# Optimization experiments

Hardware: AMD Instinct MI355X
Metric: run time of the kernel (lower is better)

The kernel has to match this reference:

```python
import jax, jax.numpy as jnp
import numpy as np

B, T, E, H, R, NTAGS, V = 128, 24, 512, 512, 512, 400, 20000

def setup_inputs() -> dict:
    key = jax.random.key(0)
    ks = jax.random.split(key, 12)
    sc = 0.03  # xavier-ish scale for 512-dim mats
    return {
        'captions': jax.random.randint(ks[0], (B, T), 0, V),
        'encoder_tags': jax.random.uniform(ks[1], (B, NTAGS), jnp.float32),
        'h0': jax.random.normal(ks[2], (2, B, H), jnp.float32),
        'c0': jax.random.normal(ks[3], (2, B, H), jnp.float32),
        'Wa': jax.random.normal(ks[4], (4, E, R), jnp.float32) * sc,
        'Wb': jax.random.normal(ks[5], (4, NTAGS, R), jnp.float32) * sc,
        'Wc': jax.random.normal(ks[6], (4, R, H), jnp.float32) * sc,
        'Ua': jax.random.normal(ks[7], (4, H, R), jnp.float32) * sc,
        'Ub': jax.random.normal(ks[8], (4, NTAGS, R), jnp.float32) * sc,
        'Uc': jax.random.normal(ks[9], (4, R, H), jnp.float32) * sc,
        'b': jnp.zeros((4, H), jnp.float32),
        'emb': jax.random.normal(ks[10], (V, E), jnp.float32) * 0.02,
        'Wout': jax.random.normal(ks[11], (H, V), jnp.float32) * sc,
        'bout': jnp.zeros((V,), jnp.float32),
    }


def reference(captions, encoder_tags, h0, c0, Wa, Wb, Wc, Ua, Ub, Uc, b, emb, Wout, bout):
    # Training branch of SCNAttnDecoder.forward_fn with teacher_forcing_ratio=1.0,
    # dropout in eval mode (identity). Gate order along leading axis 4: (i, f, o, c~).
    s = encoder_tags                                      # [B, NTAGS]
    temp2 = jnp.einsum('bt,gtr->gbr', s, Wb)              # precompute_mats: s @ Wb_*
    temp5 = jnp.einsum('bt,gtr->gbr', s, Ub)              # s @ Ub_*
    # Decoder inputs: zeros at t=0, then embedded ground-truth tokens (teacher forcing)
    emb_caps = emb[captions]                              # [B, T, E]
    xs = jnp.concatenate([jnp.zeros((captions.shape[0], 1, emb.shape[1]), emb.dtype),
                          emb_caps[:, :-1]], axis=1)
    xs = jnp.swapaxes(xs, 0, 1)                           # [T, B, E]
    # Initial state: last encoder layer, forward direction
    h_init, c_init = h0[0], c0[0]                         # [B, H]

    def step(carry, x):
        h, c = carry
        temp1 = jnp.einsum('be,ger->gbr', x, Wa)          # decoder_input @ Wa_*
        temp6 = jnp.einsum('bh,ghr->gbr', h, Ua)          # rnn_h @ Ua_*
        gx = jnp.einsum('gbr,grh->gbh', temp1 * temp2, Wc)
        gh = jnp.einsum('gbr,grh->gbh', temp5 * temp6, Uc)
        pre = gx + gh + b[:, None, :]                     # [4, B, H]
        i = jax.nn.sigmoid(pre[0])
        f = jax.nn.sigmoid(pre[1])
        o = jax.nn.sigmoid(pre[2])
        ct = jnp.tanh(pre[3])
        c_new = f * c + i * ct
        h_new = o * jnp.tanh(c_new)
        return (h_new, c_new), h_new

    (_, _), hs = jax.lax.scan(step, (h_init, c_init), xs)  # hs: [T, B, H]
    logits = jnp.einsum('tbh,hv->tbv', hs, Wout) + bout     # out Linear
    return jnp.swapaxes(logits, 0, 1)                       # [B, T, V]
```

## Files before the change

### kernel.cpp

```cpp
#include <hip/hip_runtime.h>
#include <hip/hip_bf16.h>
#include <math.h>

typedef unsigned short u16;
typedef short short8 __attribute__((ext_vector_type(8)));
typedef float floatx4 __attribute__((ext_vector_type(4)));

#define NB 128
#define NT 24
#define NE 512
#define NH 512
#define NR 512
#define NTAG 400
#define NV 20000

__device__ __forceinline__ float bfu(u16 u) {
    unsigned x = ((unsigned)u) << 16;
    return __builtin_bit_cast(float, x);
}
__device__ __forceinline__ u16 f2b(float f) {
    unsigned u = __builtin_bit_cast(unsigned, f);
    unsigned r = (u + 0x7FFFu + ((u >> 16) & 1u)) >> 16;
    return (u16)r;
}
__device__ __forceinline__ float ldin(const void* p, long i, int f32) {
    return f32 ? ((const float*)p)[i] : bfu(((const u16*)p)[i]);
}

__global__ __launch_bounds__(256) void k_detect(const void* emb, int* flag) {
    __shared__ int cnt;
    if (threadIdx.x == 0) cnt = 0;
    __syncthreads();
    const u16* p = (const u16*)emb;
    int local = 0;
    for (int i = threadIdx.x; i < 65536; i += 256) {
        if ((p[i] & 0x7F80) == 0x7F80) local++;
    }
    atomicAdd(&cnt, local);
    __syncthreads();
    if (threadIdx.x == 0) *flag = (cnt > 4) ? 1 : 0;
}

__global__ __launch_bounds__(256) void k_tags(const void* __restrict__ s,
        const void* __restrict__ Wb, const void* __restrict__ Ub,
        const int* __restrict__ flagp, float* __restrict__ temp2, float* __restrict__ temp5,
        int* __restrict__ flags) {
    if (blockIdx.x == 0 && threadIdx.x < 256) flags[threadIdx.x] = 0;
    int f32 = *flagp;
    int idx = blockIdx.x * 256 + threadIdx.x;
    int r = idx & (NR - 1);
    int gb = idx >> 9;
    int b = gb & (NB - 1);
    int g = gb >> 7;
    float a2 = 0.f, a5 = 0.f;
    if (f32) {
        const float* srow = (const float*)s + b * NTAG;
        const float* wb = (const float*)Wb + (long)g * NTAG * NR + r;
        const float* ub = (const float*)Ub + (long)g * NTAG * NR + r;
        for (int t = 0; t < NTAG; t++) {
            float sv = srow[t];
            a2 += sv * wb[(long)t * NR];
            a5 += sv * ub[(long)t * NR];
        }
    } else {
        const u16* srow = (const u16*)s + b * NTAG;
        const u16* wb = (const u16*)Wb + (long)g * NTAG * NR + r;
        const u16* ub = (const u16*)Ub + (long)g * NTAG * NR + r;
        for (int t = 0; t < NTAG; t++) {
            float sv = bfu(srow[t]);
            a2 += sv * bfu(wb[(long)t * NR]);
            a5 += sv * bfu(ub[(long)t * NR]);
        }
    }
    temp2[idx] = a2;
    temp5[idx] = a5;
}

__global__ __launch_bounds__(256) void k_tr(const void* __restrict__ Ua,
        const void* __restrict__ Uc, const int* __restrict__ flagp,
        u16* __restrict__ UaS, u16* __restrict__ UcS) {
    int f32 = *flagp;
    int z = blockIdx.z;
    int which = z >> 2, g = z & 3;
    const void* src = which ? Uc : Ua;
    u16* dst = which ? UcS : UaS;
    __shared__ u16 tile[64][65];
    int i0 = blockIdx.x * 64;
    int j0 = blockIdx.y * 64;
    int t = threadIdx.x;
    int il = t >> 2, js = (t & 3) * 16;
    long base = ((long)g * 512 + i0 + il) * 512 + j0 + js;
    if (f32) {
        const float* q = (const float*)src + base;
        #pragma unroll
        for (int j = 0; j < 16; j++) tile[il][js + j] = f2b(q[j]);
    } else {
        const u16* q = (const u16*)src + base;
        #pragma unroll
        for (int j = 0; j < 16; j++) tile[il][js + j] = q[j];
    }
    __syncthreads();
    #pragma unroll
    for (int h = 0; h < 2; h++) {
        int idx = t + h * 256;
        int kl = idx >> 6, rl = idx & 63;
        u16 outv[8] __attribute__((aligned(16)));
        #pragma unroll
        for (int j = 0; j < 8; j++) outv[j] = tile[kl * 8 + j][rl];
        long ob = ((long)(g * 64 + (i0 >> 3) + kl) * 512 + (j0 + rl)) * 8;
        *(uint4*)(dst + ob) = *(uint4*)outv;
    }
}

template<int MODE>
__global__ __launch_bounds__(256) void k_mfma(const void* __restrict__ Asrc,
        const void* __restrict__ Bsrc, void* __restrict__ dst,
        const int* __restrict__ captions, const float* __restrict__ temp2,
        const void* __restrict__ bout, const int* __restrict__ flagp) {
    const int f32 = *flagp;
    const int bm = blockIdx.x * 64;
    const int bn = blockIdx.y * 128;
    const int g = blockIdx.z;
    const int NN = (MODE == 2) ? NV : NR;
    const int ldb = (MODE == 2) ? NV : NR;
    __shared__ __align__(16) u16 As[64 * 40];
    __shared__ __align__(16) u16 Bs[32 * 132];
    const int tid = threadIdx.x;
    const int sam = tid >> 2, sak = (tid & 3) * 8;
    const int sbk = tid >> 3, sbn = (tid & 7) * 16;
    long arow = 0;
    int azero = 0;
    if (MODE == 0) {
        int mg = bm + sam, tt = mg >> 7, bb = mg & (NB - 1);
        if (tt == 0) azero = 1;
        else arow = (long)captions[bb * NT + tt - 1] * NE;
    } else if (MODE == 1) {
        arow = ((long)g * NT * NB + bm + sam) * NR;
    } else {
        arow = (long)(bm + sam) * NH;
    }
    long bbase;
    if (MODE == 2) bbase = bn + sbn;
    else bbase = (long)g * 512 * 512 + bn + sbn;
    const int bguard = (MODE == 2) && (bn + 128 > NN);

    const int wv = tid >> 6, ln = tid & 63;
    const int q = ln >> 4, l15 = ln & 15;
    floatx4 acc[4][2];
    #pragma unroll
    for (int i = 0; i < 4; i++)
        #pragma unroll
        for (int j = 0; j < 2; j++)
            #pragma unroll
            for (int r = 0; r < 4; r++) acc[i][j][r] = 0.f;

    for (int k0 = 0; k0 < 512; k0 += 32) {
        u16 ta[8] __attribute__((aligned(16)));
        if (MODE == 0) {
            if (azero) {
                #pragma unroll
                for (int j = 0; j < 8; j++) ta[j] = 0;
            } else if (f32) {
                const float* qa = (const float*)Asrc + arow + k0 + sak;
                #pragma unroll
                for (int j = 0; j < 8; j++) ta[j] = f2b(qa[j]);
            } else {
                *(uint4*)ta = *(const uint4*)((const u16*)Asrc + arow + k0 + sak);
            }
        } else {
            *(uint4*)ta = *(const uint4*)((const u16*)Asrc + arow + k0 + sak);
        }
        *(uint4*)&As[sam * 40 + sak] = *(uint4*)ta;
        u16 tb[16] __attribute__((aligned(16)));
        long be = bbase + (long)(k0 + sbk) * ldb;
        if (!bguard) {
            if (f32) {
                const float* qb = (const float*)Bsrc + be;
                #pragma unroll
                for (int j = 0; j < 16; j++) tb[j] = f2b(qb[j]);
            } else {
                *(uint4*)tb = *(const uint4*)((const u16*)Bsrc + be);
                *(uint4*)(tb + 8) = *(const uint4*)((const u16*)Bsrc + be + 8);
            }
        } else {
            #pragma unroll
            for (int j = 0; j < 16; j++) {
                int n = bn + sbn + j;
                tb[j] = (n < NN) ? (f32 ? f2b(((const float*)Bsrc)[be + j])
                                        : ((const u16*)Bsrc)[be + j]) : (u16)0;
            }
        }
        *(uint2*)&Bs[sbk * 132 + sbn]      = *(uint2*)tb;
        *(uint2*)&Bs[sbk * 132 + sbn + 4]  = *(uint2*)(tb + 4);
        *(uint2*)&Bs[sbk * 132 + sbn + 8]  = *(uint2*)(tb + 8);
        *(uint2*)&Bs[sbk * 132 + sbn + 12] = *(uint2*)(tb + 12);
        __syncthreads();
        short8 af[4];
        #pragma unroll
        for (int mi = 0; mi < 4; mi++)
            af[mi] = *(const short8*)&As[(mi * 16 + l15) * 40 + q * 8];
        #pragma unroll
        for (int ni = 0; ni < 2; ni++) {
            union { u16 u[8]; short8 v; } bu;
            int n = wv * 32 + ni * 16 + l15;
            #pragma unroll
            for (int j = 0; j < 8; j++) bu.u[j] = Bs[(q * 8 + j) * 132 + n];
            #pragma unroll
            for (int mi = 0; mi < 4; mi++)
                acc[mi][ni] = __builtin_amdgcn_mfma_f32_16x16x32_bf16(af[mi], bu.v, acc[mi][ni], 0, 0, 0);
        }
        __syncthreads();
    }
    #pragma unroll
    for (int mi = 0; mi < 4; mi++) {
        #pragma unroll
        for (int ni = 0; ni < 2; ni++) {
            int n = bn + wv * 32 + ni * 16 + l15;
            #pragma unroll
            for (int r = 0; r < 4; r++) {
                int m = bm + mi * 16 + q * 4 + r;
                float v = acc[mi][ni][r];
                if (MODE == 0) {
                    int bb = m & (NB - 1);
                    v *= temp2[((long)g * NB + bb) * NR + n];
                    ((u16*)dst)[((long)g * NT * NB + m) * NR + n] = f2b(v);
                } else if (MODE == 1) {
                    ((u16*)dst)[((long)g * NT * NB + m) * NR + n] = f2b(v);
                } else {
                    if (n < NV) {
                        int tt = m >> 7, bb = m & (NB - 1);
                        float o = v + ldin(bout, n, f32);
                        long oi = ((long)bb * NT + tt) * NV + n;
                        if (f32) ((float*)dst)[oi] = o;
                        else ((u16*)dst)[oi] = f2b(o);
                    }
                }
            }
        }
    }
}

template<bool SHARED>
__device__ __forceinline__ void dot2(const uint4* __restrict__ w0p,
        const uint4* __restrict__ w1p, const float* __restrict__ x0,
        const float* __restrict__ x1, float& o0, float& o1) {
    float a0 = 0.f, a1 = 0.f;
    uint4 c0[4], c1[4], n0[4], n1[4];
    #pragma unroll
    for (int j = 0; j < 4; j++) { c0[j] = w0p[j * 512]; c1[j] = w1p[j * 512]; }
    #pragma unroll 2
    for (int cc = 0; cc < 16; cc++) {
        if (cc < 15) {
            #pragma unroll
            for (int j = 0; j < 4; j++) {
                n0[j] = w0p[(cc * 4 + 4 + j) * 512];
                n1[j] = w1p[(cc * 4 + 4 + j) * 512];
            }
        }
        #pragma unroll
        for (int j = 0; j < 4; j++) {
            const int kb = (cc * 4 + j) * 8;
            const unsigned* p0 = (const unsigned*)&c0[j];
            const unsigned* p1 = (const unsigned*)&c1[j];
            #pragma unroll
            for (int i = 0; i < 4; i++) {
                float xl0 = x0[kb + 2 * i], xh0 = x0[kb + 2 * i + 1];
                a0 = fmaf(__builtin_bit_cast(float, p0[i] << 16), xl0, a0);
                a0 = fmaf(__builtin_bit_cast(float, p0[i] & 0xFFFF0000u), xh0, a0);
                if (SHARED) {
                    a1 = fmaf(__builtin_bit_cast(float, p1[i] << 16), xl0, a1);
                    a1 = fmaf(__builtin_bit_cast(float, p1[i] & 0xFFFF0000u), xh0, a1);
                } else {
                    float xl1 = x1[kb + 2 * i], xh1 = x1[kb + 2 * i + 1];
                    a1 = fmaf(__builtin_bit_cast(float, p1[i] << 16), xl1, a1);
                    a1 = fmaf(__builtin_bit_cast(float, p1[i] & 0xFFFF0000u), xh1, a1);
                }
            }
        }
        #pragma unroll
        for (int j = 0; j < 4; j++) { c0[j] = n0[j]; c1[j] = n1[j]; }
    }
    o0 = a0; o1 = a1;
}

__global__ __launch_bounds__(512, 2) void k_rec(const u16* __restrict__ UaS,
        const u16* __restrict__ UcS, const float* __restrict__ temp5,
        const u16* __restrict__ gx, const void* __restrict__ bias,
        const void* __restrict__ h0, const void* __restrict__ c0,
        const int* __restrict__ flagp, u16* __restrict__ hs,
        float* __restrict__ preX, int* __restrict__ flags) {
    const int f32 = *flagp;
    const int b = blockIdx.x;
    const int p = blockIdx.y;
    __shared__ __align__(16) float hf[NH];
    __shared__ __align__(16) float t6f[2 * NR];
    const int tid = threadIdx.x;
    hf[tid] = ldin(h0, (long)b * NH + tid, f32);
    float cstate = ldin(c0, (long)b * NH + tid, f32);
    const int gA = p, gB = p + 2;
    const uint4* rA0 = (const uint4*)UaS + (long)gA * 64 * 512 + tid;
    const uint4* rA1 = (const uint4*)UaS + (long)gB * 64 * 512 + tid;
    const uint4* rB0 = (const uint4*)UcS + (long)gA * 64 * 512 + tid;
    const uint4* rB1 = (const uint4*)UcS + (long)gB * 64 * 512 + tid;
    const float t5a = temp5[((long)gA * NB + b) * NR + tid];
    const float t5b = temp5[((long)gB * NB + b) * NR + tid];
    const float bia = ldin(bias, gA * NH + tid, f32);
    const float bib = ldin(bias, gB * NH + tid, f32);
    int* myFlag = &flags[b * 2 + p];
    int* otFlag = &flags[b * 2 + (1 - p)];
    __syncthreads();
    for (int t = 0; t < NT; t++) {
        float a0, a1;
        dot2<true>(rA0, rA1, hf, hf, a0, a1);
        t6f[tid] = a0 * t5a;
        t6f[NR + tid] = a1 * t5b;
        __syncthreads();
        float gxa = bfu(gx[(((long)gA * NT + t) * NB + b) * NH + tid]);
        float gxb = bfu(gx[(((long)gB * NT + t) * NB + b) * NH + tid]);
        float s0, s1;
        dot2<false>(rB0, rB1, t6f, t6f + NR, s0, s1);
        float pre0 = s0 + gxa + bia;
        float pre1 = s1 + gxb + bib;
        float* myPre = preX + ((((long)b * 2 + p) * 2 + (t & 1)) * 2) * NH;
        const float* otPre = preX + ((((long)b * 2 + (1 - p)) * 2 + (t & 1)) * 2) * NH;
        __hip_atomic_store(&myPre[tid], pre0, __ATOMIC_RELAXED, __HIP_MEMORY_SCOPE_AGENT);
        __hip_atomic_store(&myPre[NH + tid], pre1, __ATOMIC_RELAXED, __HIP_MEMORY_SCOPE_AGENT);
        __syncthreads();
        if (tid == 0) {
            __hip_atomic_store(myFlag, t + 1, __ATOMIC_RELEASE, __HIP_MEMORY_SCOPE_AGENT);
            while (__hip_atomic_load(otFlag, __ATOMIC_RELAXED, __HIP_MEMORY_SCOPE_AGENT) < t + 1)
                __builtin_amdgcn_s_sleep(2);
            __builtin_amdgcn_fence(__ATOMIC_ACQUIRE, "agent");
        }
        __syncthreads();
        float q0 = __hip_atomic_load(&otPre[tid], __ATOMIC_RELAXED, __HIP_MEMORY_SCOPE_AGENT);
        float q1 = __hip_atomic_load(&otPre[NH + tid], __ATOMIC_RELAXED, __HIP_MEMORY_SCOPE_AGENT);
        float pi, pf, po, pc;
        if (p == 0) { pi = pre0; po = pre1; pf = q0; pc = q1; }
        else        { pf = pre0; pc = pre1; pi = q0; po = q1; }
        float ig = 1.f / (1.f + expf(-pi));
        float fg = 1.f / (1.f + expf(-pf));
        float og = 1.f / (1.f + expf(-po));
        float ct = tanhf(pc);
        float cn = fg * cstate + ig * ct;
        float hn = og * tanhf(cn);
        cstate = cn;
        hf[tid] = hn;
        if (p == 0) hs[((long)t * NB + b) * NH + tid] = f2b(hn);
        __syncthreads();
    }
}

extern "C" void kernel_launch(void* const* d_in, const int* in_sizes, int n_in,
                              void* d_out, int out_size, void* d_ws, size_t ws_size,
                              hipStream_t stream) {
    const int* captions = (const int*)d_in[0];
    const void* s    = d_in[1];
    const void* h0   = d_in[2];
    const void* c0   = d_in[3];
    const void* Wa   = d_in[4];
    const void* Wb   = d_in[5];
    const void* Wc   = d_in[6];
    const void* Ua   = d_in[7];
    const void* Ub   = d_in[8];
    const void* Uc   = d_in[9];
    const void* bias = d_in[10];
    const void* emb  = d_in[11];
    const void* Wout = d_in[12];
    const void* bout = d_in[13];

    char* w = (char*)d_ws;
    int*   flag  = (int*)w;
    int*   flags = (int*)(w + 256);
    float* temp2 = (float*)(w + 2048);
    float* temp5 = temp2 + 4 * NB * NR;
    u16*   UaS   = (u16*)(temp5 + 4 * NB * NR);
    u16*   UcS   = UaS + 4 * 512 * 512;
    u16*   t1m   = UcS + 4 * 512 * 512;
    u16*   gx    = t1m + (long)4 * NT * NB * NR;
    float* preX  = (float*)(gx + (long)4 * NT * NB * NR);
    u16*   hs    = t1m;

    dim3 blk(256);
    k_detect<<<1, blk, 0, stream>>>(emb, flag);
    k_tags<<<(4 * NB * NR) / 256, blk, 0, stream>>>(s, Wb, Ub, flag, temp2, temp5, flags);
    k_tr<<<dim3(8, 8, 8), blk, 0, stream>>>(Ua, Uc, flag, UaS, UcS);

    k_mfma<0><<<dim3(48, 4, 4), blk, 0, stream>>>(emb, Wa, t1m, captions, temp2, nullptr, flag);
    k_mfma<1><<<dim3(48, 4, 4), blk, 0, stream>>>(t1m, Wc, gx, nullptr, nullptr, nullptr, flag);

    k_rec<<<dim3(128, 2), 512, 0, stream>>>(UaS, UcS, temp5, gx, bias, h0, c0, flag, hs, preX, flags);

    k_mfma<2><<<dim3(48, 157, 1), blk, 0, stream>>>(hs, Wout, d_out, nullptr, nullptr, bout, flag);
}
```

Before: 1.428 ms.

## Rewrite recurrent kernel with batched MFMA over 16-sample groups and 16-block exchange

The recurrent step kernel drops the per-sample scalar bf16 dot products, where each of 256 blocks handled one sample and half the gates. It now uses 128 blocks, each covering a 16-sample batch group, one gate and a quarter of the output columns, and computes both matmuls with bf16 MFMA 16x16x32 instructions. Gate pre-activations are exchanged through global memory with a 16-way flag barrier per batch group, and every block redundantly applies the LSTM cell update for its 16 samples. The aim is to reuse each weight read across 16 samples and to use matrix cores. In exchange, h and temp6 are now rounded to bf16, and each step needs a wider cross-block synchronisation that all 16 blocks must reach.

```diff
diff --git a/kernel.cpp b/kernel.cpp
--- a/kernel.cpp
+++ b/kernel.cpp
@@ -240,113 +240,126 @@
     }
 }
 
-template<bool SHARED>
-__device__ __forceinline__ void dot2(const uint4* __restrict__ w0p,
-        const uint4* __restrict__ w1p, const float* __restrict__ x0,
-        const float* __restrict__ x1, float& o0, float& o1) {
-    float a0 = 0.f, a1 = 0.f;
-    uint4 c0[4], c1[4], n0[4], n1[4];
-    #pragma unroll
-    for (int j = 0; j < 4; j++) { c0[j] = w0p[j * 512]; c1[j] = w1p[j * 512]; }
-    #pragma unroll 2
-    for (int cc = 0; cc < 16; cc++) {
-        if (cc < 15) {
-            #pragma unroll
-            for (int j = 0; j < 4; j++) {
-                n0[j] = w0p[(cc * 4 + 4 + j) * 512];
-                n1[j] = w1p[(cc * 4 + 4 + j) * 512];
-            }
-        }
-        #pragma unroll
-        for (int j = 0; j < 4; j++) {
-            const int kb = (cc * 4 + j) * 8;
-            const unsigned* p0 = (const unsigned*)&c0[j];
-            const unsigned* p1 = (const unsigned*)&c1[j];
-            #pragma unroll
-            for (int i = 0; i < 4; i++) {
-                float xl0 = x0[kb + 2 * i], xh0 = x0[kb + 2 * i + 1];
-                a0 = fmaf(__builtin_bit_cast(float, p0[i] << 16), xl0, a0);
-                a0 = fmaf(__builtin_bit_cast(float, p0[i] & 0xFFFF0000u), xh0, a0);
-                if (SHARED) {
-                    a1 = fmaf(__builtin_bit_cast(float, p1[i] << 16), xl0, a1);
-                    a1 = fmaf(__builtin_bit_cast(float, p1[i] & 0xFFFF0000u), xh0, a1);
-                } else {
-                    float xl1 = x1[kb + 2 * i], xh1 = x1[kb + 2 * i + 1];
-                    a1 = fmaf(__builtin_bit_cast(float, p1[i] << 16), xl1, a1);
-                    a1 = fmaf(__builtin_bit_cast(float, p1[i] & 0xFFFF0000u), xh1, a1);
-                }
-            }
-        }
-        #pragma unroll
-        for (int j = 0; j < 4; j++) { c0[j] = n0[j]; c1[j] = n1[j]; }
-    }
-    o0 = a0; o1 = a1;
-}
-
-__global__ __launch_bounds__(512, 2) void k_rec(const u16* __restrict__ UaS,
+__global__ __launch_bounds__(512) void k_rec(const u16* __restrict__ UaS,
         const u16* __restrict__ UcS, const float* __restrict__ temp5,
         const u16* __restrict__ gx, const void* __restrict__ bias,
         const void* __restrict__ h0, const void* __restrict__ c0,
         const int* __restrict__ flagp, u16* __restrict__ hs,
         float* __restrict__ preX, int* __restrict__ flags) {
     const int f32 = *flagp;
-    const int b = blockIdx.x;
-    const int p = blockIdx.y;
-    __shared__ __align__(16) float hf[NH];
-    __shared__ __align__(16) float t6f[2 * NR];
+    const int bid = blockIdx.x;
+    const int bg = bid >> 4;
+    const int g  = (bid >> 2) & 3;
+    const int c  = bid & 3;
+    const int myid = g * 4 + c;
     const int tid = threadIdx.x;
-    hf[tid] = ldin(h0, (long)b * NH + tid, f32);
-    float cstate = ldin(c0, (long)b * NH + tid, f32);
-    const int gA = p, gB = p + 2;
-    const uint4* rA0 = (const uint4*)UaS + (long)gA * 64 * 512 + tid;
-    const uint4* rA1 = (const uint4*)UaS + (long)gB * 64 * 512 + tid;
-    const uint4* rB0 = (const uint4*)UcS + (long)gA * 64 * 512 + tid;
-    const uint4* rB1 = (const uint4*)UcS + (long)gB * 64 * 512 + tid;
-    const float t5a = temp5[((long)gA * NB + b) * NR + tid];
-    const float t5b = temp5[((long)gB * NB + b) * NR + tid];
-    const float bia = ldin(bias, gA * NH + tid, f32);
-    const float bib = ldin(bias, gB * NH + tid, f32);
-    int* myFlag = &flags[b * 2 + p];
-    int* otFlag = &flags[b * 2 + (1 - p)];
+    const int wv = tid >> 6, ln = tid & 63, q = ln >> 4, l15 = ln & 15;
+
+    __shared__ __align__(16) u16 hb[16 * 520];
+    __shared__ __align__(16) u16 t6s[16 * 520];
+
+    const int pb = tid >> 5;
+    const int pj = (tid & 31) * 16;
+    const int bglob = bg * 16 + pb;
+    float cs[16];
+    #pragma unroll
+    for (int j = 0; j < 16; j++) {
+        hb[pb * 520 + pj + j] = f2b(ldin(h0, (long)bglob * NH + pj + j, f32));
+        cs[j] = ldin(c0, (long)bglob * NH + pj + j, f32);
+    }
+    float t5v[4][4];
+    #pragma unroll
+    for (int nt = 0; nt < 4; nt++)
+        #pragma unroll
+        for (int r = 0; r < 4; r++)
+            t5v[nt][r] = temp5[((long)g * NB + bg * 16 + q * 4 + r) * NR
+                               + wv * 64 + nt * 16 + l15];
+    const bool own = (myid == (pj >> 5));
     __syncthreads();
+
     for (int t = 0; t < NT; t++) {
-        float a0, a1;
-        dot2<true>(rA0, rA1, hf, hf, a0, a1);
-        t6f[tid] = a0 * t5a;
-        t6f[NR + tid] = a1 * t5b;
-        __syncthreads();
-        float gxa = bfu(gx[(((long)gA * NT + t) * NB + b) * NH + tid]);
-        float gxb = bfu(gx[(((long)gB * NT + t) * NB + b) * NH + tid]);
-        float s0, s1;
-        dot2<false>(rB0, rB1, t6f, t6f + NR, s0, s1);
-        float pre0 = s0 + gxa + bia;
-        float pre1 = s1 + gxb + bib;
-        float* myPre = preX + ((((long)b * 2 + p) * 2 + (t & 1)) * 2) * NH;
-        const float* otPre = preX + ((((long)b * 2 + (1 - p)) * 2 + (t & 1)) * 2) * NH;
-        __hip_atomic_store(&myPre[tid], pre0, __ATOMIC_RELAXED, __HIP_MEMORY_SCOPE_AGENT);
-        __hip_atomic_store(&myPre[NH + tid], pre1, __ATOMIC_RELAXED, __HIP_MEMORY_SCOPE_AGENT);
-        __syncthreads();
-        if (tid == 0) {
-            __hip_atomic_store(myFlag, t + 1, __ATOMIC_RELEASE, __HIP_MEMORY_SCOPE_AGENT);
-            while (__hip_atomic_load(otFlag, __ATOMIC_RELAXED, __HIP_MEMORY_SCOPE_AGENT) < t + 1)
-                __builtin_amdgcn_s_sleep(2);
-            __builtin_amdgcn_fence(__ATOMIC_ACQUIRE, "agent");
-        }
-        __syncthreads();
-        float q0 = __hip_atomic_load(&otPre[tid], __ATOMIC_RELAXED, __HIP_MEMORY_SCOPE_AGENT);
-        float q1 = __hip_atomic_load(&otPre[NH + tid], __ATOMIC_RELAXED, __HIP_MEMORY_SCOPE_AGENT);
-        float pi, pf, po, pc;
-        if (p == 0) { pi = pre0; po = pre1; pf = q0; pc = q1; }
-        else        { pf = pre0; pc = pre1; pi = q0; po = q1; }
-        float ig = 1.f / (1.f + expf(-pi));
-        float fg = 1.f / (1.f + expf(-pf));
-        float og = 1.f / (1.f + expf(-po));
-        float ct = tanhf(pc);
-        float cn = fg * cstate + ig * ct;
-        float hn = og * tanhf(cn);
-        cstate = cn;
-        hf[tid] = hn;
-        if (p == 0) hs[((long)t * NB + b) * NH + tid] = f2b(hn);
+        const int pr_ = t & 1;
+        floatx4 accA[4];
+        #pragma unroll
+        for (int nt = 0; nt < 4; nt++)
+            #pragma unroll
+            for (int r = 0; r < 4; r++) accA[nt][r] = 0.f;
+        const int colA = wv * 64 + l15;
+        #pragma unroll 4
+        for (int ks = 0; ks < 16; ks++) {
+            short8 af = *(const short8*)&hb[l15 * 520 + ks * 32 + q * 8];
+            #pragma unroll
+            for (int nt = 0; nt < 4; nt++) {
+                short8 bf = *(const short8*)(UaS
+                    + ((long)(g * 64 + ks * 4 + q) * 512 + colA + nt * 16) * 8);
+                accA[nt] = __builtin_amdgcn_mfma_f32_16x16x32_bf16(af, bf, accA[nt], 0, 0, 0);
+            }
+        }
+        #pragma unroll
+        for (int nt = 0; nt < 4; nt++)
+            #pragma unroll
+            for (int r = 0; r < 4; r++)
+                t6s[(q * 4 + r) * 520 + colA + nt * 16] = f2b(accA[nt][r] * t5v[nt][r]);
+        __syncthreads();
+        floatx4 accB;
+        #pragma unroll
+        for (int r = 0; r < 4; r++) accB[r] = 0.f;
+        const int colB = c * 128 + wv * 16 + l15;
+        #pragma unroll 4
+        for (int ks = 0; ks < 16; ks++) {
+            short8 af = *(const short8*)&t6s[l15 * 520 + ks * 32 + q * 8];
+            short8 bf = *(const short8*)(UcS
+                + ((long)(g * 64 + ks * 4 + q) * 512 + colB) * 8);
+            accB = __builtin_amdgcn_mfma_f32_16x16x32_bf16(af, bf, accB, 0, 0, 0);
+        }
+        float* pbase = preX + (((long)pr_ * 8 + bg) * 4 + g) * 16 * 512;
+        #pragma unroll
+        for (int r = 0; r < 4; r++)
+            __hip_atomic_store(&pbase[(q * 4 + r) * 512 + colB], accB[r],
+                               __ATOMIC_RELAXED, __HIP_MEMORY_SCOPE_AGENT);
+        __syncthreads();
+        if (tid == 0)
+            __hip_atomic_store(&flags[bg * 16 + myid], t + 1,
+                               __ATOMIC_RELEASE, __HIP_MEMORY_SCOPE_AGENT);
+        if (tid < 16)
+            while (__hip_atomic_load(&flags[bg * 16 + tid],
+                       __ATOMIC_RELAXED, __HIP_MEMORY_SCOPE_AGENT) < t + 1)
+                __builtin_amdgcn_s_sleep(1);
+        __syncthreads();
+        __builtin_amdgcn_fence(__ATOMIC_ACQUIRE, "agent");
+        float pv[4][16];
+        #pragma unroll
+        for (int g4 = 0; g4 < 4; g4++) {
+            const float* pbg = preX + ((((long)pr_ * 8 + bg) * 4 + g4) * 16 + pb) * 512 + pj;
+            union { uint4 v[2]; u16 u[16]; } gxu;
+            const u16* gp = gx + (((long)g4 * NT + t) * NB + bglob) * NH + pj;
+            gxu.v[0] = *(const uint4*)gp;
+            gxu.v[1] = *(const uint4*)(gp + 8);
+            #pragma unroll
+            for (int j = 0; j < 16; j++)
+                pv[g4][j] = __hip_atomic_load(&pbg[j], __ATOMIC_RELAXED,
+                                              __HIP_MEMORY_SCOPE_AGENT)
+                            + bfu(gxu.u[j]) + ldin(bias, g4 * NH + pj + j, f32);
+        }
+        union { uint4 v[2]; u16 u[16]; } ho;
+        #pragma unroll
+        for (int j = 0; j < 16; j++) {
+            float ig = 1.f / (1.f + expf(-pv[0][j]));
+            float fg = 1.f / (1.f + expf(-pv[1][j]));
+            float og = 1.f / (1.f + expf(-pv[2][j]));
+            float ct = tanhf(pv[3][j]);
+            float cn = fg * cs[j] + ig * ct;
+            float hn = og * tanhf(cn);
+            cs[j] = cn;
+            ho.u[j] = f2b(hn);
+        }
+        *(uint4*)&hb[pb * 520 + pj]     = ho.v[0];
+        *(uint4*)&hb[pb * 520 + pj + 8] = ho.v[1];
+        if (own) {
+            uint4* hp = (uint4*)&hs[((long)t * NB + bglob) * NH + pj];
+            hp[0] = ho.v[0];
+            hp[1] = ho.v[1];
+        }
         __syncthreads();
     }
 }
@@ -389,7 +402,7 @@
     k_mfma<0><<<dim3(48, 4, 4), blk, 0, stream>>>(emb, Wa, t1m, captions, temp2, nullptr, flag);
     k_mfma<1><<<dim3(48, 4, 4), blk, 0, stream>>>(t1m, Wc, gx, nullptr, nullptr, nullptr, flag);
 
-    k_rec<<<dim3(128, 2), 512, 0, stream>>>(UaS, UcS, temp5, gx, bias, h0, c0, flag, hs, preX, flags);
+    k_rec<<<128, 512, 0, stream>>>(UaS, UcS, temp5, gx, bias, h0, c0, flag, hs, preX, flags);
 
     k_mfma<2><<<dim3(48, 157, 1), blk, 0, stream>>>(hs, Wout, d_out, nullptr, nullptr, bout, flag);
 }
```

New measurement: 2.111 ms. 1.48x slower.
